# Optimization experiments

Hardware: AMD Instinct MI355X
Metric: run time of the kernel (lower is better)

## Reference

```python
import jax, jax.numpy as jnp
import numpy as np

N = 100000      # nodes
E = 1600000     # edges (avg degree 16)
NFEAT = 128
NHID = 128
LRELU_SLOPE = 0.2

def setup_inputs() -> dict:
    key = jax.random.key(0)
    ks = jax.random.split(key, 12)
    s = 1.0 / np.sqrt(NFEAT)
    inp = {}
    inp["x"] = jax.random.normal(ks[0], (N, NFEAT), dtype=jnp.float32)
    inp["edge_row"] = jax.random.randint(ks[1], (E,), 0, N, dtype=jnp.int32)
    inp["edge_col"] = jax.random.randint(ks[2], (E,), 0, N, dtype=jnp.int32)
    inp["edge_val"] = jax.random.uniform(ks[3], (E,), dtype=jnp.float32)
    inp["norm"] = jax.random.uniform(ks[4], (N, 1), dtype=jnp.float32) * 16.0 + 1.0
    # Relation params (bias-free Linears, torch layout y = x @ W.T)
    inp["Wg1"] = jax.random.uniform(ks[5], (NFEAT, NFEAT), minval=-s, maxval=s, dtype=jnp.float32)
    inp["Wg2"] = jax.random.uniform(ks[6], (NFEAT, NFEAT), minval=-s, maxval=s, dtype=jnp.float32)
    inp["Wb1"] = jax.random.uniform(ks[7], (NFEAT, NFEAT), minval=-s, maxval=s, dtype=jnp.float32)
    inp["Wb2"] = jax.random.uniform(ks[8], (NFEAT, NFEAT), minval=-s, maxval=s, dtype=jnp.float32)
    inp["r"] = jax.random.uniform(ks[9], (1, NFEAT), minval=-s, maxval=s, dtype=jnp.float32)
    # GraphConv weight [nfeat, nhid]
    inp["gc_w"] = jax.random.uniform(ks[10], (NFEAT, NHID), minval=-s, maxval=s, dtype=jnp.float32)
    return inp

def _spmm(edge_row, edge_col, edge_val, h):
    # sparse [N,N] @ dense [N,D] via gather + segment-sum
    return jax.ops.segment_sum(edge_val[:, None] * h[edge_col], edge_row, num_segments=N)

def reference(x, edge_row, edge_col, edge_val, norm, Wg1, Wg2, Wb1, Wb2, r, gc_w):
    # neighbor = sp.mm(adj, x)
    neighbor = _spmm(edge_row, edge_col, edge_val, x)
    # Relation (ver=1, ablation=0): FiLM-modulated transE relation vector
    gamma = jax.nn.leaky_relu(x @ Wg1.T + neighbor @ Wg2.T, LRELU_SLOPE) + 1.0
    beta = jax.nn.leaky_relu(x @ Wb1.T + neighbor @ Wb2.T, LRELU_SLOPE)
    m = x + (gamma * r + beta) - neighbor
    # tail branch (head=False, ablation=0): h_s = m @ gc.weight
    h_s = m @ gc_w
    # GraphConv with adj_self = adj + I (no norm inside)
    xw = x @ gc_w
    h_k = _spmm(edge_row, edge_col, edge_val, xw) + xw
    h_k = (h_k + h_s) / (norm + 1.0)
    return (h_k, m)
```

## Files before the change

### kernel.cpp

```cpp
#include <hip/hip_runtime.h>

#define N_NODES 100000
#define NFEAT 128
#define E_EDGES 1600000
#define LRELU_SLOPE 0.2f
#define BM 32
#define NB2 3125
#define SCAP 2048
#define HB_BLOCKS 256
#define HB_PER 6250
#define XB_BLOCKS 3125
#define PK_BLOCKS 320

typedef short bf16x8 __attribute__((ext_vector_type(8)));
typedef float f32x4 __attribute__((ext_vector_type(4)));

__device__ __forceinline__ ushort f2bf(float f) {
    union { float f; uint u; } v; v.f = f;
    uint u = v.u;
    return (ushort)((u + 0x7fffu + ((u >> 16) & 1u)) >> 16);
}
__device__ __forceinline__ float bf2f(ushort s) {
    union { uint u; float f; } v; v.u = ((uint)s) << 16;
    return v.f;
}
__device__ __forceinline__ float blo(uint u) {
    union { uint u; float f; } v; v.u = u << 16; return v.f;
}
__device__ __forceinline__ float bhi(uint u) {
    union { uint u; float f; } v; v.u = u & 0xFFFF0000u; return v.f;
}

__global__ __launch_bounds__(256) void mega_prep(
    const int* __restrict__ er, int* __restrict__ ghist,
    const float* __restrict__ x, ushort* __restrict__ xb,
    const float* __restrict__ Wg1, const float* __restrict__ Wg2,
    const float* __restrict__ Wb1, const float* __restrict__ Wb2,
    const float* __restrict__ gcw,
    ushort* __restrict__ W1p, ushort* __restrict__ W2p)
{
    __shared__ int hist[NB2];
    const int bid = blockIdx.x;
    const int tid = threadIdx.x;

    if (bid < HB_BLOCKS) {
        for (int k = tid; k < NB2; k += 256) hist[k] = 0;
        __syncthreads();
        const int e0 = bid * HB_PER;
        for (int k = tid; k < HB_PER; k += 256)
            atomicAdd(&hist[er[e0 + k] >> 5], 1);
        __syncthreads();
        for (int k = tid; k < NB2; k += 256) ghist[bid * NB2 + k] = hist[k];
    } else if (bid < HB_BLOCKS + XB_BLOCKS) {
        size_t base = ((size_t)(bid - HB_BLOCKS) * 256 + tid) * 16;
        float4 a = *reinterpret_cast<const float4*>(x + base);
        float4 b = *reinterpret_cast<const float4*>(x + base + 4);
        float4 c = *reinterpret_cast<const float4*>(x + base + 8);
        float4 d = *reinterpret_cast<const float4*>(x + base + 12);
        uint4 o1, o2;
        o1.x = (uint)f2bf(a.x) | ((uint)f2bf(a.y) << 16);
        o1.y = (uint)f2bf(a.z) | ((uint)f2bf(a.w) << 16);
        o1.z = (uint)f2bf(b.x) | ((uint)f2bf(b.y) << 16);
        o1.w = (uint)f2bf(b.z) | ((uint)f2bf(b.w) << 16);
        o2.x = (uint)f2bf(c.x) | ((uint)f2bf(c.y) << 16);
        o2.y = (uint)f2bf(c.z) | ((uint)f2bf(c.w) << 16);
        o2.z = (uint)f2bf(d.x) | ((uint)f2bf(d.y) << 16);
        o2.w = (uint)f2bf(d.z) | ((uint)f2bf(d.w) << 16);
        *reinterpret_cast<uint4*>(xb + base) = o1;
        *reinterpret_cast<uint4*>(xb + base + 8) = o2;
    } else {
        int idx = (bid - HB_BLOCKS - XB_BLOCKS) * 256 + tid;
        if (idx < 65536) {
            int jj = idx & 7;
            int lane = (idx >> 3) & 63;
            int tile = idx >> 9;
            int nt = tile & 15, kt = tile >> 4;
            int k = kt * 32 + (lane >> 4) * 8 + jj;
            int j = nt * 16 + (lane & 15);
            float v;
            if (j < 128) v = (k < 128) ? Wg1[j * 128 + k] : Wg2[j * 128 + (k - 128)];
            else { int c = j - 128; v = (k < 128) ? Wb1[c * 128 + k] : Wb2[c * 128 + (k - 128)]; }
            W1p[idx] = f2bf(v);
        } else if (idx < 81920) {
            int i2 = idx - 65536;
            int jj = i2 & 7;
            int lane = (i2 >> 3) & 63;
            int tile = i2 >> 9;
            int nt = tile & 7, kt = tile >> 3;
            int k = kt * 32 + (lane >> 4) * 8 + jj;
            int j = nt * 16 + (lane & 15);
            W2p[i2] = f2bf(gcw[k * 128 + j]);
        }
    }
}

__global__ __launch_bounds__(256) void scan_hist(
    const int* __restrict__ ghist, int* __restrict__ gbase,
    int* __restrict__ cursorB)
{
    int c = blockIdx.x * 256 + threadIdx.x;
    if (c >= NB2) return;
    int acc = c * SCAP;
#pragma unroll 8
    for (int r = 0; r < HB_BLOCKS; r++) {
        gbase[r * NB2 + c] = acc;
        acc += ghist[r * NB2 + c];
    }
    cursorB[c] = acc - c * SCAP;
}

__global__ __launch_bounds__(512) void scatter_edges(
    const int* __restrict__ er, const int* __restrict__ ec,
    const float* __restrict__ ev, const int* __restrict__ gbase,
    int2* __restrict__ stg)
{
    __shared__ int cur[NB2];
    const int bid = blockIdx.x;
    const int tid = threadIdx.x;
    for (int k = tid; k < NB2; k += 512) cur[k] = gbase[bid * NB2 + k];
    __syncthreads();
    const int e0 = bid * HB_PER;
#pragma unroll 2
    for (int k = tid; k < HB_PER; k += 512) {
        int e = e0 + k;
        int r = er[e];
        int t = atomicAdd(&cur[r >> 5], 1);
        int2 o;
        o.x = (ec[e] << 13) | (r & 31);
        o.y = __float_as_int(ev[e]);
        stg[t] = o;
    }
}

__global__ __launch_bounds__(512, 8) void fused_all(
    const int* __restrict__ cursorB, const int2* stg,
    const ushort* __restrict__ xb,
    const float* __restrict__ norm, const float* __restrict__ rvec,
    const ushort* __restrict__ W1p, const ushort* __restrict__ W2p,
    float* hk, float* __restrict__ mout)
{
    __shared__ ushort SM[16384];
    __shared__ int h32[32], rs32[32], pd32[32], cur32[32];
    char* asb = (char*)SM;
    char* gbb = (char*)(SM + 8192);
    int2* elist = (int2*)gbb;

    const int tid = threadIdx.x;
    const int lane = tid & 63;
    const int w = tid >> 6;
    const int g = lane >> 4;
    const int s = lane & 15;
    const int b = blockIdx.x;
    const int node0 = b * BM;

    {
        int rr = tid >> 4;
        int cq = tid & 15;
        uint4 v = *reinterpret_cast<const uint4*>(xb + (size_t)(node0 + rr) * 128 + cq * 8);
        *(uint4*)(asb + ((rr * 512 + cq * 16) ^ ((rr & 7) << 4))) = v;
    }

    const int cntE = cursorB[b];
    const int2* sb = stg + (size_t)b * SCAP;
    int2 E0, E1;
    const bool v0 = tid < cntE, v1 = tid + 512 < cntE;
    if (v0) E0 = sb[tid];
    if (v1) E1 = sb[tid + 512];
    if (tid < 32) h32[tid] = 0;
    __syncthreads();
    if (v0) atomicAdd(&h32[E0.x & 31], 1);
    if (v1) atomicAdd(&h32[E1.x & 31], 1);
    __syncthreads();
    if (tid < 64) {
        int pc = 0;
        if (tid < 32) { int h = h32[tid]; pc = (h + 7) & ~7; cur32[tid] = 0; }
        int v = pc;
        for (int off = 1; off < 32; off <<= 1) {
            int t = __shfl_up(v, off, 64);
            if (lane >= off) v += t;
        }
        if (tid < 32) { rs32[tid] = v - pc; pd32[tid] = pc; }
    }
    __syncthreads();
    if (v0) { int rl = E0.x & 31; elist[rs32[rl] + atomicAdd(&cur32[rl], 1)] = E0; }
    if (v1) { int rl = E1.x & 31; elist[rs32[rl] + atomicAdd(&cur32[rl], 1)] = E1; }
    if (tid < 32) {
        int rs = rs32[tid];
        for (int j = h32[tid]; j < pd32[tid]; ++j) elist[rs + j] = make_int2(tid, 0);
    }
    __syncthreads();

    const char* xbase = (const char*)xb + s * 16;
#pragma unroll 1
    for (int i = 0; i < 4; i++) {
        int rr = w * 4 + i;
        const int2* el = elist + rs32[rr];
        int pd = pd32[rr];
        float ac0 = 0.f, ac1 = 0.f, ac2 = 0.f, ac3 = 0.f;
        float ac4 = 0.f, ac5 = 0.f, ac6 = 0.f, ac7 = 0.f;
#pragma unroll 2
        for (int j = 0; j < pd; j += 8) {
            int2 e0 = el[j + g];
            int2 e1 = el[j + 4 + g];
            uint4 q0 = *reinterpret_cast<const uint4*>(xbase + (e0.x >> 5));
            uint4 q1 = *reinterpret_cast<const uint4*>(xbase + (e1.x >> 5));
            float f0 = __int_as_float(e0.y);
            float f1 = __int_as_float(e1.y);
            ac0 += f0 * blo(q0.x); ac1 += f0 * bhi(q0.x);
            ac2 += f0 * blo(q0.y); ac3 += f0 * bhi(q0.y);
            ac4 += f0 * blo(q0.z); ac5 += f0 * bhi(q0.z);
            ac6 += f0 * blo(q0.w); ac7 += f0 * bhi(q0.w);
            ac0 += f1 * blo(q1.x); ac1 += f1 * bhi(q1.x);
            ac2 += f1 * blo(q1.y); ac3 += f1 * bhi(q1.y);
            ac4 += f1 * blo(q1.z); ac5 += f1 * bhi(q1.z);
            ac6 += f1 * blo(q1.w); ac7 += f1 * bhi(q1.w);
        }
        ac0 += __shfl_xor(ac0, 16, 64); ac0 += __shfl_xor(ac0, 32, 64);
        ac1 += __shfl_xor(ac1, 16, 64); ac1 += __shfl_xor(ac1, 32, 64);
        ac2 += __shfl_xor(ac2, 16, 64); ac2 += __shfl_xor(ac2, 32, 64);
        ac3 += __shfl_xor(ac3, 16, 64); ac3 += __shfl_xor(ac3, 32, 64);
        ac4 += __shfl_xor(ac4, 16, 64); ac4 += __shfl_xor(ac4, 32, 64);
        ac5 += __shfl_xor(ac5, 16, 64); ac5 += __shfl_xor(ac5, 32, 64);
        ac6 += __shfl_xor(ac6, 16, 64); ac6 += __shfl_xor(ac6, 32, 64);
        ac7 += __shfl_xor(ac7, 16, 64); ac7 += __shfl_xor(ac7, 32, 64);
        if (g == 0) {
            uint4 o;
            o.x = (uint)f2bf(ac0) | ((uint)f2bf(ac1) << 16);
            o.y = (uint)f2bf(ac2) | ((uint)f2bf(ac3) << 16);
            o.z = (uint)f2bf(ac4) | ((uint)f2bf(ac5) << 16);
            o.w = (uint)f2bf(ac6) | ((uint)f2bf(ac7) << 16);
            *(uint4*)(asb + ((rr * 512 + 256 + s * 16) ^ ((rr & 7) << 4))) = o;
        }
    }
    __syncthreads();

    f32x4 acc[2][2];
#pragma unroll
    for (int mt = 0; mt < 2; mt++)
#pragma unroll
        for (int nl = 0; nl < 2; nl++) acc[mt][nl] = (f32x4){0.f, 0.f, 0.f, 0.f};

#pragma unroll
    for (int kt = 0; kt < 8; kt++) {
        bf16x8 af[2];
#pragma unroll
        for (int mt = 0; mt < 2; mt++) {
            int row = mt * 16 + (lane & 15);
            int off = (row * 512 + kt * 64 + (lane >> 4) * 16) ^ ((row & 7) << 4);
            af[mt] = *(bf16x8*)(asb + off);
        }
#pragma unroll
        for (int nl = 0; nl < 2; nl++) {
            int nt = w * 2 + nl;
            bf16x8 bfg = *(const bf16x8*)(W1p + (((kt * 16 + nt) * 64 + lane) << 3));
#pragma unroll
            for (int mt = 0; mt < 2; mt++)
                acc[mt][nl] = __builtin_amdgcn_mfma_f32_16x16x32_bf16(af[mt], bfg, acc[mt][nl], 0, 0, 0);
        }
    }

#pragma unroll
    for (int mt = 0; mt < 2; mt++)
#pragma unroll
        for (int nl = 0; nl < 2; nl++) {
            int j = (w * 2 + nl) * 16 + (lane & 15);
#pragma unroll
            for (int reg = 0; reg < 4; reg++) {
                int row = mt * 16 + (lane >> 4) * 4 + reg;
                int off = (row * 512 + j * 2) ^ ((row & 7) << 4);
                *(ushort*)(gbb + off) = f2bf(acc[mt][nl][reg]);
            }
        }
    __syncthreads();

    {
        int c = tid & 127;
        float rv = rvec[c];
        int rg = tid >> 7;
#pragma unroll 4
        for (int i = 0; i < 8; i++) {
            int row = rg * 8 + i;
            int swz = (row & 7) << 4;
            int bx = (row * 512 + c * 2) ^ swz;
            int bn = (row * 512 + 256 + c * 2) ^ swz;
            float graw = bf2f(*(ushort*)(gbb + bx));
            float braw = bf2f(*(ushort*)(gbb + bn));
            float xv = bf2f(*(ushort*)(asb + bx));
            float nv = bf2f(*(ushort*)(asb + bn));
            float gamma = ((graw > 0.f) ? graw : LRELU_SLOPE * graw) + 1.f;
            float beta = (braw > 0.f) ? braw : LRELU_SLOPE * braw;
            float gb_ = gamma * rv + beta;
            float mv = xv + gb_ - nv;
            float tv = 2.f * xv + gb_;
            mout[(size_t)(node0 + row) * 128 + c] = mv;
            *(ushort*)(asb + bx) = f2bf(tv);
        }
    }
    __syncthreads();

    f32x4 acc2[2];
#pragma unroll
    for (int mt = 0; mt < 2; mt++) acc2[mt] = (f32x4){0.f, 0.f, 0.f, 0.f};

#pragma unroll
    for (int kt = 0; kt < 4; kt++) {
        bf16x8 af[2];
#pragma unroll
        for (int mt = 0; mt < 2; mt++) {
            int row = mt * 16 + (lane & 15);
            int off = (row * 512 + kt * 64 + (lane >> 4) * 16) ^ ((row & 7) << 4);
            af[mt] = *(bf16x8*)(asb + off);
        }
        bf16x8 bfg = *(const bf16x8*)(W2p + (((kt * 8 + w) * 64 + lane) << 3));
#pragma unroll
        for (int mt = 0; mt < 2; mt++)
            acc2[mt] = __builtin_amdgcn_mfma_f32_16x16x32_bf16(af[mt], bfg, acc2[mt], 0, 0, 0);
    }

#pragma unroll
    for (int mt = 0; mt < 2; mt++) {
        int col = w * 16 + (lane & 15);
#pragma unroll
        for (int reg = 0; reg < 4; reg++) {
            int row = mt * 16 + (lane >> 4) * 4 + reg;
            int node = node0 + row;
            float inv = 1.f / (norm[node] + 1.f);
            hk[(size_t)node * 128 + col] = acc2[mt][reg] * inv;
        }
    }
}

extern "C" void kernel_launch(void* const* d_in, const int* in_sizes, int n_in,
                              void* d_out, int out_size, void* d_ws, size_t ws_size,
                              hipStream_t stream)
{
    const float* x    = (const float*)d_in[0];
    const int*   er   = (const int*)d_in[1];
    const int*   ec   = (const int*)d_in[2];
    const float* ev   = (const float*)d_in[3];
    const float* norm = (const float*)d_in[4];
    const float* Wg1  = (const float*)d_in[5];
    const float* Wg2  = (const float*)d_in[6];
    const float* Wb1  = (const float*)d_in[7];
    const float* Wb2  = (const float*)d_in[8];
    const float* r    = (const float*)d_in[9];
    const float* gcw  = (const float*)d_in[10];

    float* out  = (float*)d_out;
    float* hk   = out;
    float* mout = out + (size_t)N_NODES * NFEAT;

    ushort* xb      = (ushort*)d_ws;
    ushort* W1p     = xb + (size_t)N_NODES * NFEAT;
    ushort* W2p     = W1p + 65536;
    int*    cursorB = (int*)(W2p + 16384);
    int*    ghist   = cursorB + NB2;
    int*    gbase   = ghist + HB_BLOCKS * NB2;

    int2* stg = (int2*)hk;

    mega_prep<<<HB_BLOCKS + XB_BLOCKS + PK_BLOCKS, 256, 0, stream>>>(
        er, ghist, x, xb, Wg1, Wg2, Wb1, Wb2, gcw, W1p, W2p);

    scan_hist<<<(NB2 + 255) / 256, 256, 0, stream>>>(ghist, gbase, cursorB);

    scatter_edges<<<HB_BLOCKS, 512, 0, stream>>>(er, ec, ev, gbase, stg);

    fused_all<<<NB2, 512, 0, stream>>>(
        cursorB, stg, xb, norm, r, W1p, W2p, hk, mout);
}
```

Before: 155.4 us.

## Parallelize histogram scan into two passes and software-prefetch MFMA weight fragments

Replaces the single serial column scan over 256 histogram rows (only 3125 threads) with a two-pass scan split into 16 partitions, using the output buffer as scratch for the partial sums. Weight fragments for both MFMA loops are now prefetched two k-steps ahead in registers, and edge staging loads are issued unconditionally at kernel start to hide latency. Unroll factors are raised on the histogram and scatter loops. This adds a kernel launch and more register pressure, and it reads stg entries past the valid count.

```diff
diff --git a/kernel.cpp b/kernel.cpp
--- a/kernel.cpp
+++ b/kernel.cpp
@@ -11,6 +11,7 @@
 #define HB_PER 6250
 #define XB_BLOCKS 3125
 #define PK_BLOCKS 320
+#define SCAN_P 16
 
 typedef short bf16x8 __attribute__((ext_vector_type(8)));
 typedef float f32x4 __attribute__((ext_vector_type(4)));
@@ -47,6 +48,7 @@
         for (int k = tid; k < NB2; k += 256) hist[k] = 0;
         __syncthreads();
         const int e0 = bid * HB_PER;
+#pragma unroll 4
         for (int k = tid; k < HB_PER; k += 256)
             atomicAdd(&hist[er[e0 + k] >> 5], 1);
         __syncthreads();
@@ -94,19 +96,33 @@
     }
 }
 
-__global__ __launch_bounds__(256) void scan_hist(
-    const int* __restrict__ ghist, int* __restrict__ gbase,
-    int* __restrict__ cursorB)
-{
-    int c = blockIdx.x * 256 + threadIdx.x;
-    if (c >= NB2) return;
-    int acc = c * SCAP;
-#pragma unroll 8
-    for (int r = 0; r < HB_BLOCKS; r++) {
-        gbase[r * NB2 + c] = acc;
-        acc += ghist[r * NB2 + c];
-    }
-    cursorB[c] = acc - c * SCAP;
+__global__ __launch_bounds__(256) void scan_s(
+    const int* __restrict__ ghist, int* __restrict__ S)
+{
+    int t = blockIdx.x * 256 + threadIdx.x;
+    if (t >= SCAN_P * NB2) return;
+    int c = t % NB2, p = t / NB2;
+    int acc = 0;
+#pragma unroll
+    for (int r = p * 16; r < p * 16 + 16; r++) acc += ghist[r * NB2 + c];
+    S[p * NB2 + c] = acc;
+}
+
+__global__ __launch_bounds__(256) void scan_w(
+    const int* __restrict__ ghist, const int* __restrict__ S,
+    int* __restrict__ gbase, int* __restrict__ cursorB)
+{
+    int t = blockIdx.x * 256 + threadIdx.x;
+    if (t >= SCAN_P * NB2) return;
+    int c = t % NB2, p = t / NB2;
+    int base = c * SCAP;
+    for (int q = 0; q < p; q++) base += S[q * NB2 + c];
+#pragma unroll
+    for (int r = p * 16; r < p * 16 + 16; r++) {
+        gbase[r * NB2 + c] = base;
+        base += ghist[r * NB2 + c];
+    }
+    if (p == SCAN_P - 1) cursorB[c] = base - c * SCAP;
 }
 
 __global__ __launch_bounds__(512) void scatter_edges(
@@ -120,7 +136,7 @@
     for (int k = tid; k < NB2; k += 512) cur[k] = gbase[bid * NB2 + k];
     __syncthreads();
     const int e0 = bid * HB_PER;
-#pragma unroll 2
+#pragma unroll 4
     for (int k = tid; k < HB_PER; k += 512) {
         int e = e0 + k;
         int r = er[e];
@@ -153,6 +169,11 @@
     const int b = blockIdx.x;
     const int node0 = b * BM;
 
+    const int2* sb = stg + (size_t)b * SCAP;
+    int2 E0 = sb[tid];
+    int2 E1 = sb[tid + 512];
+    const int cntE = cursorB[b];
+
     {
         int rr = tid >> 4;
         int cq = tid & 15;
@@ -160,12 +181,7 @@
         *(uint4*)(asb + ((rr * 512 + cq * 16) ^ ((rr & 7) << 4))) = v;
     }
 
-    const int cntE = cursorB[b];
-    const int2* sb = stg + (size_t)b * SCAP;
-    int2 E0, E1;
     const bool v0 = tid < cntE, v1 = tid + 512 < cntE;
-    if (v0) E0 = sb[tid];
-    if (v1) E1 = sb[tid + 512];
     if (tid < 32) h32[tid] = 0;
     __syncthreads();
     if (v0) atomicAdd(&h32[E0.x & 31], 1);
@@ -232,6 +248,10 @@
             *(uint4*)(asb + ((rr * 512 + 256 + s * 16) ^ ((rr & 7) << 4))) = o;
         }
     }
+
+    #define W1L(kt, nl) (*(const bf16x8*)(W1p + ((((kt) * 16 + w * 2 + (nl)) * 64 + lane) << 3)))
+    bf16x8 wc0 = W1L(0, 0), wc1 = W1L(0, 1);
+    bf16x8 wn0 = W1L(1, 0), wn1 = W1L(1, 1);
     __syncthreads();
 
     f32x4 acc[2][2];
@@ -242,6 +262,8 @@
 
 #pragma unroll
     for (int kt = 0; kt < 8; kt++) {
+        bf16x8 wf0, wf1;
+        if (kt < 6) { wf0 = W1L(kt + 2, 0); wf1 = W1L(kt + 2, 1); }
         bf16x8 af[2];
 #pragma unroll
         for (int mt = 0; mt < 2; mt++) {
@@ -250,14 +272,14 @@
             af[mt] = *(bf16x8*)(asb + off);
         }
 #pragma unroll
-        for (int nl = 0; nl < 2; nl++) {
-            int nt = w * 2 + nl;
-            bf16x8 bfg = *(const bf16x8*)(W1p + (((kt * 16 + nt) * 64 + lane) << 3));
-#pragma unroll
-            for (int mt = 0; mt < 2; mt++)
-                acc[mt][nl] = __builtin_amdgcn_mfma_f32_16x16x32_bf16(af[mt], bfg, acc[mt][nl], 0, 0, 0);
-        }
-    }
+        for (int mt = 0; mt < 2; mt++) {
+            acc[mt][0] = __builtin_amdgcn_mfma_f32_16x16x32_bf16(af[mt], wc0, acc[mt][0], 0, 0, 0);
+            acc[mt][1] = __builtin_amdgcn_mfma_f32_16x16x32_bf16(af[mt], wc1, acc[mt][1], 0, 0, 0);
+        }
+        wc0 = wn0; wc1 = wn1;
+        if (kt < 6) { wn0 = wf0; wn1 = wf1; }
+    }
+    #undef W1L
 
 #pragma unroll
     for (int mt = 0; mt < 2; mt++)
@@ -296,6 +318,10 @@
             *(ushort*)(asb + bx) = f2bf(tv);
         }
     }
+
+    #define W2L(kt) (*(const bf16x8*)(W2p + ((((kt) * 8 + w) * 64 + lane) << 3)))
+    bf16x8 vc = W2L(0);
+    bf16x8 vn = W2L(1);
     __syncthreads();
 
     f32x4 acc2[2];
@@ -304,6 +330,8 @@
 
 #pragma unroll
     for (int kt = 0; kt < 4; kt++) {
+        bf16x8 vf;
+        if (kt < 2) vf = W2L(kt + 2);
         bf16x8 af[2];
 #pragma unroll
         for (int mt = 0; mt < 2; mt++) {
@@ -311,11 +339,13 @@
             int off = (row * 512 + kt * 64 + (lane >> 4) * 16) ^ ((row & 7) << 4);
             af[mt] = *(bf16x8*)(asb + off);
         }
-        bf16x8 bfg = *(const bf16x8*)(W2p + (((kt * 8 + w) * 64 + lane) << 3));
 #pragma unroll
         for (int mt = 0; mt < 2; mt++)
-            acc2[mt] = __builtin_amdgcn_mfma_f32_16x16x32_bf16(af[mt], bfg, acc2[mt], 0, 0, 0);
-    }
+            acc2[mt] = __builtin_amdgcn_mfma_f32_16x16x32_bf16(af[mt], vc, acc2[mt], 0, 0, 0);
+        vc = vn;
+        if (kt < 2) vn = vf;
+    }
+    #undef W2L
 
 #pragma unroll
     for (int mt = 0; mt < 2; mt++) {
@@ -357,12 +387,15 @@
     int*    ghist   = cursorB + NB2;
     int*    gbase   = ghist + HB_BLOCKS * NB2;
 
+    int*  S   = (int*)mout;
     int2* stg = (int2*)hk;
 
     mega_prep<<<HB_BLOCKS + XB_BLOCKS + PK_BLOCKS, 256, 0, stream>>>(
         er, ghist, x, xb, Wg1, Wg2, Wb1, Wb2, gcw, W1p, W2p);
 
-    scan_hist<<<(NB2 + 255) / 256, 256, 0, stream>>>(ghist, gbase, cursorB);
+    scan_s<<<(SCAN_P * NB2 + 255) / 256, 256, 0, stream>>>(ghist, S);
+
+    scan_w<<<(SCAN_P * NB2 + 255) / 256, 256, 0, stream>>>(ghist, S, gbase, cursorB);
 
     scatter_edges<<<HB_BLOCKS, 512, 0, stream>>>(er, ec, ev, gbase, stg);
 
```

After: 153.2 us. No clear change (-1.4%).
